# Kernel tuning notes

Hardware: AMD Instinct MI355X
Metric: run time of the kernel (lower is better)

The kernel has to match this reference:

```python
import jax, jax.numpy as jnp
import numpy as np

N = 4096
D = 512
H = 3


def setup_inputs() -> dict:
    key = jax.random.key(0)
    k1, k2, k3 = jax.random.split(key, 3)
    graph_info = (jax.random.uniform(k1, (N, N)) < 0.01).astype(jnp.float32)
    h = jax.random.normal(k2, (N, D), dtype=jnp.float32)
    # xavier_normal_ with relu gain: std = sqrt(2) * sqrt(2/(fan_in+fan_out))
    std = np.sqrt(2.0) * np.sqrt(2.0 / (D + H))
    P = jax.random.normal(k3, (D, H), dtype=jnp.float32) * jnp.float32(std)
    return {"graph_info": graph_info, "h": h, "P": P}


def reference(graph_info, h, P):
    # graph_info_1 = spmm(graph_info^T, I)^T == graph_info (identity densification)
    mask = graph_info > 0                                  # [N, N]
    E = jax.nn.relu(h @ P)                                 # [N, H] per-node scores, all heads
    NEG = jnp.float32(-9e15)
    # e is broadcast along rows: att[i, j] = E[j, k] where edge (i->j) exists
    logits = jnp.where(mask[None, :, :], E.T[:, None, :], NEG)  # [H, N, N]
    att = jax.nn.softmax(logits, axis=-1)                  # row-softmax per head
    hh = jnp.einsum('hij,jd->hid', att, h)                 # [H, N, D] aggregate
    # sum_flag == 1: scale each row i by its degree (rowsum of graph_info_1)
    rowsum = jnp.sum(graph_info, axis=-1)                  # [N]
    hh = hh * rowsum[None, :, None]
    # multi_head > 1, concat=False: sum over heads
    return jnp.sum(hh, axis=0)                             # [N, D]
```

## Files before the change

### kernel.cpp

```cpp
#include <hip/hip_runtime.h>
#include <stdint.h>

#define NN 4096
#define DD 512
#define NH 3
#define MAXDEG 256

typedef float f4v __attribute__((ext_vector_type(4)));

__device__ __forceinline__ unsigned short f2bf_rn(float x) {
    union { float f; uint32_t u; } v; v.f = x;
    uint32_t u = v.u;
    uint32_t r = (u + 0x7FFFu + ((u >> 16) & 1u)) >> 16;
    return (unsigned short)r;
}
__device__ __forceinline__ float bflo(uint32_t u) {
    union { uint32_t u; float f; } v; v.u = u << 16; return v.f;
}
__device__ __forceinline__ float bfhi(uint32_t u) {
    union { uint32_t u; float f; } v; v.u = u & 0xFFFF0000u; return v.f;
}

__global__ __launch_bounds__(256) void prep_kernel(
    const float* __restrict__ h, const float* __restrict__ P,
    float* __restrict__ w, unsigned short* __restrict__ hb)
{
    int gid = blockIdx.x * 256 + threadIdx.x;
    int row = gid >> 6, ln = gid & 63;
    const f4v* h4 = (const f4v*)(h + (size_t)row * DD);
    f4v va = __builtin_nontemporal_load(&h4[ln * 2]);
    f4v vb = __builtin_nontemporal_load(&h4[ln * 2 + 1]);
    float e[8] = { va[0], va[1], va[2], va[3], vb[0], vb[1], vb[2], vb[3] };

    uint32_t pk0 = (uint32_t)f2bf_rn(e[0]) | ((uint32_t)f2bf_rn(e[1]) << 16);
    uint32_t pk1 = (uint32_t)f2bf_rn(e[2]) | ((uint32_t)f2bf_rn(e[3]) << 16);
    uint32_t pk2 = (uint32_t)f2bf_rn(e[4]) | ((uint32_t)f2bf_rn(e[5]) << 16);
    uint32_t pk3 = (uint32_t)f2bf_rn(e[6]) | ((uint32_t)f2bf_rn(e[7]) << 16);
    uint4 pk = make_uint4(pk0, pk1, pk2, pk3);
    *(uint4*)(hb + (size_t)row * DD + ln * 8) = pk;

    int d0 = ln * 8;
    float a0 = 0.f, a1 = 0.f, a2 = 0.f;
    #pragma unroll
    for (int k = 0; k < 8; ++k) {
        float hv = e[k];
        const float* Pr = P + (size_t)(d0 + k) * NH;
        a0 = fmaf(hv, Pr[0], a0);
        a1 = fmaf(hv, Pr[1], a1);
        a2 = fmaf(hv, Pr[2], a2);
    }
    #pragma unroll
    for (int off = 32; off > 0; off >>= 1) {
        a0 += __shfl_down(a0, off);
        a1 += __shfl_down(a1, off);
        a2 += __shfl_down(a2, off);
    }
    if (ln == 0) {
        w[row * NH + 0] = expf(fmaxf(a0, 0.f));
        w[row * NH + 1] = expf(fmaxf(a1, 0.f));
        w[row * NH + 2] = expf(fmaxf(a2, 0.f));
    }
}

__global__ __launch_bounds__(256) void att_agg_kernel(
    const float* __restrict__ g, const unsigned short* __restrict__ hb,
    const float* __restrict__ w, float* __restrict__ out)
{
    __shared__ int   s_idx[4][MAXDEG + 8];
    __shared__ float s_c[4][MAXDEG + 8];

    const int wv = threadIdx.x >> 6, ln = threadIdx.x & 63;
    const int row = blockIdx.x * 4 + wv;
    int*   __restrict__ idxb = s_idx[wv];
    float* __restrict__ cb   = s_c[wv];

    const f4v* g4 = (const f4v*)(g + (size_t)row * NN);
    int cnt = 0;
    #pragma unroll 4
    for (int it = 0; it < (NN / 4) / 64; ++it) {
        f4v v = __builtin_nontemporal_load(&g4[it * 64 + ln]);
        int base = (it * 64 + ln) * 4;
        #pragma unroll
        for (int k = 0; k < 4; ++k) {
            bool p = v[k] > 0.f;
            unsigned long long m = __ballot(p);
            if (m) {
                if (p) {
                    unsigned pre = __builtin_amdgcn_mbcnt_lo((unsigned)m, 0u);
                    pre = __builtin_amdgcn_mbcnt_hi((unsigned)(m >> 32), pre);
                    int pos = cnt + (int)pre;
                    if (pos < MAXDEG) idxb[pos] = base + k;
                }
                cnt += __popcll(m);
            }
        }
    }
    int nnz = cnt > MAXDEG ? MAXDEG : cnt;

    float* orow = out + (size_t)row * DD + ln * 8;
    if (nnz == 0) {
        f4v z = {0.f, 0.f, 0.f, 0.f};
        __builtin_nontemporal_store(z, (f4v*)orow);
        __builtin_nontemporal_store(z, (f4v*)(orow + 4));
        return;
    }

    __builtin_amdgcn_wave_barrier();

    float z0 = 0.f, z1 = 0.f, z2 = 0.f;
    for (int t = ln; t < nnz; t += 64) {
        int j = idxb[t];
        const float* wr = w + (size_t)j * NH;
        z0 += wr[0]; z1 += wr[1]; z2 += wr[2];
    }
    #pragma unroll
    for (int off = 32; off > 0; off >>= 1) {
        z0 += __shfl_xor(z0, off);
        z1 += __shfl_xor(z1, off);
        z2 += __shfl_xor(z2, off);
    }
    float RS = (float)nnz;
    float sc0 = RS / z0, sc1 = RS / z1, sc2 = RS / z2;

    int npad = (nnz + 3) & ~3;
    for (int t = ln; t < npad; t += 64) {
        if (t < nnz) {
            int j = idxb[t];
            const float* wr = w + (size_t)j * NH;
            cb[t] = fmaf(sc0, wr[0], fmaf(sc1, wr[1], sc2 * wr[2]));
        } else {
            idxb[t] = idxb[0];
            cb[t] = 0.f;
        }
    }
    __builtin_amdgcn_wave_barrier();

    const unsigned short* hcol = hb + ln * 8;
    float acc0=0.f,acc1=0.f,acc2=0.f,acc3=0.f,acc4=0.f,acc5=0.f,acc6=0.f,acc7=0.f;
    for (int t = 0; t < npad; t += 4) {
        int j0 = idxb[t+0]; float c0 = cb[t+0];
        int j1 = idxb[t+1]; float c1 = cb[t+1];
        int j2 = idxb[t+2]; float c2 = cb[t+2];
        int j3 = idxb[t+3]; float c3 = cb[t+3];
        uint4 r0 = *(const uint4*)(hcol + (size_t)j0 * DD);
        uint4 r1 = *(const uint4*)(hcol + (size_t)j1 * DD);
        uint4 r2 = *(const uint4*)(hcol + (size_t)j2 * DD);
        uint4 r3 = *(const uint4*)(hcol + (size_t)j3 * DD);
        acc0 = fmaf(c0, bflo(r0.x), acc0); acc1 = fmaf(c0, bfhi(r0.x), acc1);
        acc2 = fmaf(c0, bflo(r0.y), acc2); acc3 = fmaf(c0, bfhi(r0.y), acc3);
        acc4 = fmaf(c0, bflo(r0.z), acc4); acc5 = fmaf(c0, bfhi(r0.z), acc5);
        acc6 = fmaf(c0, bflo(r0.w), acc6); acc7 = fmaf(c0, bfhi(r0.w), acc7);
        acc0 = fmaf(c1, bflo(r1.x), acc0); acc1 = fmaf(c1, bfhi(r1.x), acc1);
        acc2 = fmaf(c1, bflo(r1.y), acc2); acc3 = fmaf(c1, bfhi(r1.y), acc3);
        acc4 = fmaf(c1, bflo(r1.z), acc4); acc5 = fmaf(c1, bfhi(r1.z), acc5);
        acc6 = fmaf(c1, bflo(r1.w), acc6); acc7 = fmaf(c1, bfhi(r1.w), acc7);
        acc0 = fmaf(c2, bflo(r2.x), acc0); acc1 = fmaf(c2, bfhi(r2.x), acc1);
        acc2 = fmaf(c2, bflo(r2.y), acc2); acc3 = fmaf(c2, bfhi(r2.y), acc3);
        acc4 = fmaf(c2, bflo(r2.z), acc4); acc5 = fmaf(c2, bfhi(r2.z), acc5);
        acc6 = fmaf(c2, bflo(r2.w), acc6); acc7 = fmaf(c2, bfhi(r2.w), acc7);
        acc0 = fmaf(c3, bflo(r3.x), acc0); acc1 = fmaf(c3, bfhi(r3.x), acc1);
        acc2 = fmaf(c3, bflo(r3.y), acc2); acc3 = fmaf(c3, bfhi(r3.y), acc3);
        acc4 = fmaf(c3, bflo(r3.z), acc4); acc5 = fmaf(c3, bfhi(r3.z), acc5);
        acc6 = fmaf(c3, bflo(r3.w), acc6); acc7 = fmaf(c3, bfhi(r3.w), acc7);
    }

    f4v o0 = {acc0, acc1, acc2, acc3};
    f4v o1 = {acc4, acc5, acc6, acc7};
    __builtin_nontemporal_store(o0, (f4v*)orow);
    __builtin_nontemporal_store(o1, (f4v*)(orow + 4));
}

extern "C" void kernel_launch(void* const* d_in, const int* in_sizes, int n_in,
                              void* d_out, int out_size, void* d_ws, size_t ws_size,
                              hipStream_t stream) {
    const float* g = (const float*)d_in[0];
    const float* h = (const float*)d_in[1];
    const float* P = (const float*)d_in[2];
    float* out = (float*)d_out;

    float* w = (float*)d_ws;
    unsigned short* hb = (unsigned short*)((char*)d_ws + 65536);

    prep_kernel<<<(NN * 64) / 256, 256, 0, stream>>>(h, P, w, hb);
    att_agg_kernel<<<NN / 4, 256, 0, stream>>>(g, hb, w, out);
}
```

Before: 118.0 us.

## Split each adjacency row across four waves with block-level edge list merge

Each block now handles a single row instead of four. Its four waves each scan a quarter of the row's adjacency, compacting neighbour indices into per-wave segments, and the segments are merged in shared memory into one (index, coefficient) list. All four waves then gather over the same edge list, each producing a 128-column slice of the output with 8-way unrolled 4-byte bf16 loads. This exposes more memory-level parallelism, since there are four times as many blocks and four independent row loads are issued up front. In exchange it adds block barriers, issues narrower gather loads, and caps each quarter at 80 neighbours, which could truncate denser rows.

```diff
diff --git a/kernel.cpp b/kernel.cpp
--- a/kernel.cpp
+++ b/kernel.cpp
@@ -4,9 +4,11 @@
 #define NN 4096
 #define DD 512
 #define NH 3
-#define MAXDEG 256
+#define SEGCAP 80
+#define MAXDEG (4 * SEGCAP)
 
 typedef float f4v __attribute__((ext_vector_type(4)));
+typedef float f2v __attribute__((ext_vector_type(2)));
 
 __device__ __forceinline__ unsigned short f2bf_rn(float x) {
     union { float f; uint32_t u; } v; v.f = x;
@@ -62,54 +64,69 @@
     }
 }
 
-__global__ __launch_bounds__(256) void att_agg_kernel(
+__global__ __launch_bounds__(256, 8) void att_agg_kernel(
     const float* __restrict__ g, const unsigned short* __restrict__ hb,
     const float* __restrict__ w, float* __restrict__ out)
 {
-    __shared__ int   s_idx[4][MAXDEG + 8];
-    __shared__ float s_c[4][MAXDEG + 8];
+    __shared__ int   s_seg[4][SEGCAP];
+    __shared__ int2  s_f[MAXDEG + 8];
+    __shared__ int   s_cnt[4];
+    __shared__ float s_z[4][3];
 
     const int wv = threadIdx.x >> 6, ln = threadIdx.x & 63;
-    const int row = blockIdx.x * 4 + wv;
-    int*   __restrict__ idxb = s_idx[wv];
-    float* __restrict__ cb   = s_c[wv];
-
-    const f4v* g4 = (const f4v*)(g + (size_t)row * NN);
+    const int row = blockIdx.x;
+
+    const f4v* g4 = (const f4v*)(g + (size_t)row * NN + wv * 1024);
+    f4v v0 = __builtin_nontemporal_load(&g4[0 * 64 + ln]);
+    f4v v1 = __builtin_nontemporal_load(&g4[1 * 64 + ln]);
+    f4v v2 = __builtin_nontemporal_load(&g4[2 * 64 + ln]);
+    f4v v3 = __builtin_nontemporal_load(&g4[3 * 64 + ln]);
+
     int cnt = 0;
-    #pragma unroll 4
-    for (int it = 0; it < (NN / 4) / 64; ++it) {
-        f4v v = __builtin_nontemporal_load(&g4[it * 64 + ln]);
-        int base = (it * 64 + ln) * 4;
-        #pragma unroll
-        for (int k = 0; k < 4; ++k) {
-            bool p = v[k] > 0.f;
-            unsigned long long m = __ballot(p);
-            if (m) {
-                if (p) {
-                    unsigned pre = __builtin_amdgcn_mbcnt_lo((unsigned)m, 0u);
-                    pre = __builtin_amdgcn_mbcnt_hi((unsigned)(m >> 32), pre);
-                    int pos = cnt + (int)pre;
-                    if (pos < MAXDEG) idxb[pos] = base + k;
-                }
-                cnt += __popcll(m);
-            }
-        }
-    }
-    int nnz = cnt > MAXDEG ? MAXDEG : cnt;
-
-    float* orow = out + (size_t)row * DD + ln * 8;
+    #define SCAN4(VV, U)                                                     \
+    {                                                                        \
+        int base = wv * 1024 + ((U) * 64 + ln) * 4;                          \
+        _Pragma("unroll")                                                    \
+        for (int k = 0; k < 4; ++k) {                                        \
+            bool p = (VV)[k] > 0.f;                                          \
+            unsigned long long m = __ballot(p);                              \
+            if (m) {                                                         \
+                if (p) {                                                     \
+                    unsigned pre = __builtin_amdgcn_mbcnt_lo((unsigned)m, 0u); \
+                    pre = __builtin_amdgcn_mbcnt_hi((unsigned)(m >> 32), pre); \
+                    int pos = cnt + (int)pre;                                \
+                    if (pos < SEGCAP) s_seg[wv][pos] = base + k;             \
+                }                                                            \
+                cnt += __popcll(m);                                          \
+            }                                                                \
+        }                                                                    \
+    }
+    SCAN4(v0, 0) SCAN4(v1, 1) SCAN4(v2, 2) SCAN4(v3, 3)
+    #undef SCAN4
+    if (cnt > SEGCAP) cnt = SEGCAP;
+    if (ln == 0) s_cnt[wv] = cnt;
+    __syncthreads();
+
+    const int c0n = s_cnt[0], c1n = s_cnt[1], c2n = s_cnt[2], c3n = s_cnt[3];
+    const int nnz = c0n + c1n + c2n + c3n;
+    float* oq = out + (size_t)row * DD + wv * 128 + ln * 2;
+
     if (nnz == 0) {
-        f4v z = {0.f, 0.f, 0.f, 0.f};
-        __builtin_nontemporal_store(z, (f4v*)orow);
-        __builtin_nontemporal_store(z, (f4v*)(orow + 4));
+        f2v z = {0.f, 0.f};
+        __builtin_nontemporal_store(z, (f2v*)oq);
         return;
     }
 
-    __builtin_amdgcn_wave_barrier();
-
     float z0 = 0.f, z1 = 0.f, z2 = 0.f;
-    for (int t = ln; t < nnz; t += 64) {
-        int j = idxb[t];
+    int myj = 0; float w0 = 0.f, w1 = 0.f, w2 = 0.f;
+    if (ln < cnt) {
+        myj = s_seg[wv][ln];
+        const float* wr = w + (size_t)myj * NH;
+        w0 = wr[0]; w1 = wr[1]; w2 = wr[2];
+        z0 = w0; z1 = w1; z2 = w2;
+    }
+    for (int t = 64 + ln; t < cnt; t += 64) {
+        int j = s_seg[wv][t];
         const float* wr = w + (size_t)j * NH;
         z0 += wr[0]; z1 += wr[1]; z2 += wr[2];
     }
@@ -119,55 +136,62 @@
         z1 += __shfl_xor(z1, off);
         z2 += __shfl_xor(z2, off);
     }
-    float RS = (float)nnz;
-    float sc0 = RS / z0, sc1 = RS / z1, sc2 = RS / z2;
-
-    int npad = (nnz + 3) & ~3;
-    for (int t = ln; t < npad; t += 64) {
-        if (t < nnz) {
-            int j = idxb[t];
-            const float* wr = w + (size_t)j * NH;
-            cb[t] = fmaf(sc0, wr[0], fmaf(sc1, wr[1], sc2 * wr[2]));
-        } else {
-            idxb[t] = idxb[0];
-            cb[t] = 0.f;
-        }
-    }
-    __builtin_amdgcn_wave_barrier();
-
-    const unsigned short* hcol = hb + ln * 8;
-    float acc0=0.f,acc1=0.f,acc2=0.f,acc3=0.f,acc4=0.f,acc5=0.f,acc6=0.f,acc7=0.f;
-    for (int t = 0; t < npad; t += 4) {
-        int j0 = idxb[t+0]; float c0 = cb[t+0];
-        int j1 = idxb[t+1]; float c1 = cb[t+1];
-        int j2 = idxb[t+2]; float c2 = cb[t+2];
-        int j3 = idxb[t+3]; float c3 = cb[t+3];
-        uint4 r0 = *(const uint4*)(hcol + (size_t)j0 * DD);
-        uint4 r1 = *(const uint4*)(hcol + (size_t)j1 * DD);
-        uint4 r2 = *(const uint4*)(hcol + (size_t)j2 * DD);
-        uint4 r3 = *(const uint4*)(hcol + (size_t)j3 * DD);
-        acc0 = fmaf(c0, bflo(r0.x), acc0); acc1 = fmaf(c0, bfhi(r0.x), acc1);
-        acc2 = fmaf(c0, bflo(r0.y), acc2); acc3 = fmaf(c0, bfhi(r0.y), acc3);
-        acc4 = fmaf(c0, bflo(r0.z), acc4); acc5 = fmaf(c0, bfhi(r0.z), acc5);
-        acc6 = fmaf(c0, bflo(r0.w), acc6); acc7 = fmaf(c0, bfhi(r0.w), acc7);
-        acc0 = fmaf(c1, bflo(r1.x), acc0); acc1 = fmaf(c1, bfhi(r1.x), acc1);
-        acc2 = fmaf(c1, bflo(r1.y), acc2); acc3 = fmaf(c1, bfhi(r1.y), acc3);
-        acc4 = fmaf(c1, bflo(r1.z), acc4); acc5 = fmaf(c1, bfhi(r1.z), acc5);
-        acc6 = fmaf(c1, bflo(r1.w), acc6); acc7 = fmaf(c1, bfhi(r1.w), acc7);
-        acc0 = fmaf(c2, bflo(r2.x), acc0); acc1 = fmaf(c2, bfhi(r2.x), acc1);
-        acc2 = fmaf(c2, bflo(r2.y), acc2); acc3 = fmaf(c2, bfhi(r2.y), acc3);
-        acc4 = fmaf(c2, bflo(r2.z), acc4); acc5 = fmaf(c2, bfhi(r2.z), acc5);
-        acc6 = fmaf(c2, bflo(r2.w), acc6); acc7 = fmaf(c2, bfhi(r2.w), acc7);
-        acc0 = fmaf(c3, bflo(r3.x), acc0); acc1 = fmaf(c3, bfhi(r3.x), acc1);
-        acc2 = fmaf(c3, bflo(r3.y), acc2); acc3 = fmaf(c3, bfhi(r3.y), acc3);
-        acc4 = fmaf(c3, bflo(r3.z), acc4); acc5 = fmaf(c3, bfhi(r3.z), acc5);
-        acc6 = fmaf(c3, bflo(r3.w), acc6); acc7 = fmaf(c3, bfhi(r3.w), acc7);
-    }
-
-    f4v o0 = {acc0, acc1, acc2, acc3};
-    f4v o1 = {acc4, acc5, acc6, acc7};
-    __builtin_nontemporal_store(o0, (f4v*)orow);
-    __builtin_nontemporal_store(o1, (f4v*)(orow + 4));
+    if (ln == 0) { s_z[wv][0] = z0; s_z[wv][1] = z1; s_z[wv][2] = z2; }
+    __syncthreads();
+
+    const float Z0 = s_z[0][0] + s_z[1][0] + s_z[2][0] + s_z[3][0];
+    const float Z1 = s_z[0][1] + s_z[1][1] + s_z[2][1] + s_z[3][1];
+    const float Z2 = s_z[0][2] + s_z[1][2] + s_z[2][2] + s_z[3][2];
+    const float RS = (float)nnz;
+    const float sc0 = RS / Z0, sc1 = RS / Z1, sc2 = RS / Z2;
+
+    const int off0 = (wv > 0 ? c0n : 0) + (wv > 1 ? c1n : 0) + (wv > 2 ? c2n : 0);
+    if (ln < cnt) {
+        float c = fmaf(sc0, w0, fmaf(sc1, w1, sc2 * w2));
+        s_f[off0 + ln] = make_int2(myj, __float_as_int(c));
+    }
+    for (int t = 64 + ln; t < cnt; t += 64) {
+        int j = s_seg[wv][t];
+        const float* wr = w + (size_t)j * NH;
+        float c = fmaf(sc0, wr[0], fmaf(sc1, wr[1], sc2 * wr[2]));
+        s_f[off0 + t] = make_int2(j, __float_as_int(c));
+    }
+    const int npad = (nnz + 7) & ~7;
+    if (wv == 0) {
+        for (int t = nnz + ln; t < npad; t += 64)
+            s_f[t] = make_int2(0, 0);
+    }
+    __syncthreads();
+
+    const unsigned short* hq = hb + wv * 128 + ln * 2;
+    float a0 = 0.f, a1 = 0.f;
+    for (int t = 0; t < npad; t += 8) {
+        int2 f0 = s_f[t + 0], f1 = s_f[t + 1], f2 = s_f[t + 2], f3 = s_f[t + 3];
+        int2 f4 = s_f[t + 4], f5 = s_f[t + 5], f6 = s_f[t + 6], f7 = s_f[t + 7];
+        uint32_t r0 = *(const uint32_t*)(hq + (size_t)f0.x * DD);
+        uint32_t r1 = *(const uint32_t*)(hq + (size_t)f1.x * DD);
+        uint32_t r2 = *(const uint32_t*)(hq + (size_t)f2.x * DD);
+        uint32_t r3 = *(const uint32_t*)(hq + (size_t)f3.x * DD);
+        uint32_t r4 = *(const uint32_t*)(hq + (size_t)f4.x * DD);
+        uint32_t r5 = *(const uint32_t*)(hq + (size_t)f5.x * DD);
+        uint32_t r6 = *(const uint32_t*)(hq + (size_t)f6.x * DD);
+        uint32_t r7 = *(const uint32_t*)(hq + (size_t)f7.x * DD);
+        float c0 = __int_as_float(f0.y), c1 = __int_as_float(f1.y);
+        float c2 = __int_as_float(f2.y), c3 = __int_as_float(f3.y);
+        float c4 = __int_as_float(f4.y), c5 = __int_as_float(f5.y);
+        float c6 = __int_as_float(f6.y), c7 = __int_as_float(f7.y);
+        a0 = fmaf(c0, bflo(r0), a0); a1 = fmaf(c0, bfhi(r0), a1);
+        a0 = fmaf(c1, bflo(r1), a0); a1 = fmaf(c1, bfhi(r1), a1);
+        a0 = fmaf(c2, bflo(r2), a0); a1 = fmaf(c2, bfhi(r2), a1);
+        a0 = fmaf(c3, bflo(r3), a0); a1 = fmaf(c3, bfhi(r3), a1);
+        a0 = fmaf(c4, bflo(r4), a0); a1 = fmaf(c4, bfhi(r4), a1);
+        a0 = fmaf(c5, bflo(r5), a0); a1 = fmaf(c5, bfhi(r5), a1);
+        a0 = fmaf(c6, bflo(r6), a0); a1 = fmaf(c6, bfhi(r6), a1);
+        a0 = fmaf(c7, bflo(r7), a0); a1 = fmaf(c7, bfhi(r7), a1);
+    }
+
+    f2v o = {a0, a1};
+    __builtin_nontemporal_store(o, (f2v*)oq);
 }
 
 extern "C" void kernel_launch(void* const* d_in, const int* in_sizes, int n_in,
@@ -182,5 +206,5 @@
     unsigned short* hb = (unsigned short*)((char*)d_ws + 65536);
 
     prep_kernel<<<(NN * 64) / 256, 256, 0, stream>>>(h, P, w, hb);
-    att_agg_kernel<<<NN / 4, 256, 0, stream>>>(g, hb, w, out);
-}
+    att_agg_kernel<<<NN, 256, 0, stream>>>(g, hb, w, out);
+}
```

After: 118.8 us. About the same (+0.7%).
